# Performance work log

Measured on AMD Instinct MI355X. Metric: run time of the kernel, lower is better.

The kernel has to match this reference:

```python
import jax, jax.numpy as jnp
import numpy as np

B, NQ, K = 256, 16, 200           # batch, num_neg+1, num_keys
KEY_SIZE, QUERY_SIZE, HIDDEN = 64, 64, 128
NEG_INF_SCALE = -1000000000.0


def setup_inputs() -> dict:
    key = jax.random.key(0)
    ks = jax.random.split(key, 9)
    queries = jax.random.normal(ks[0], (B, NQ, QUERY_SIZE), dtype=jnp.float32)
    keys = jax.random.normal(ks[1], (B, K, KEY_SIZE), dtype=jnp.float32)
    cum_subs_masks = (jax.random.uniform(ks[2], (B, NQ, K, 1)) < 0.3).astype(jnp.float32)
    s = 1.0 / np.sqrt(HIDDEN)
    Wq = jax.random.normal(ks[3], (QUERY_SIZE, HIDDEN), dtype=jnp.float32) * s
    bq = jnp.zeros((HIDDEN,), dtype=jnp.float32)
    Wk = jax.random.normal(ks[4], (KEY_SIZE, HIDDEN), dtype=jnp.float32) * s
    bk = jnp.zeros((HIDDEN,), dtype=jnp.float32)
    Wv = jax.random.normal(ks[5], (HIDDEN, 1), dtype=jnp.float32) * s
    bv = jnp.zeros((1,), dtype=jnp.float32)
    return {"queries": queries, "keys": keys, "cum_subs_masks": cum_subs_masks,
            "num_neg": NQ - 1, "Wq": Wq, "bq": bq, "Wk": Wk, "bk": bk,
            "Wv": Wv, "bv": bv}


def reference(queries, keys, cum_subs_masks, num_neg, Wq, bq, Wk, bk, Wv, bv):
    # project once, broadcast instead of expanding keys per query (same math)
    qh = queries @ Wq + bq                 # (B, NQ, H)
    kh = keys @ Wk + bk                    # (B, K, H)
    h = jnp.tanh(qh[:, :, None, :] + kh[:, None, :, :])   # (B, NQ, K, H)
    scores = h @ Wv + bv                   # (B, NQ, K, 1)
    if cum_subs_masks is not None:
        scores = scores + cum_subs_masks * NEG_INF_SCALE
    attn_weight = jax.nn.softmax(scores, axis=-2)          # softmax over keys
    attn_out = jnp.sum(attn_weight * keys[:, None, :, :], axis=-2)  # (B, NQ, key_size)
    return (attn_out, attn_weight)
```

## Files before the change

### kernel.cpp

```cpp
#include <hip/hip_runtime.h>
#include <hip/hip_bf16.h>

namespace {

typedef __attribute__((ext_vector_type(8))) short short8;
typedef __attribute__((ext_vector_type(4))) float f32x4;

constexpr int kNB = 256;
constexpr int kNQ = 16;
constexpr int kNK = 200;
constexpr int kDK = 64;
constexpr int kNH = 128;
constexpr int kThreads = 1024;
constexpr int kS = 132;
constexpr float kNeg = -1000000000.0f;
constexpr float kC2 = 2.8853900817779268f;

constexpr int kKhFloats = kNK * kS;
constexpr int kScFloats = kNQ * kNK;
constexpr int kQhFloats = kNQ * kNH;
constexpr size_t kSmemBytes =
    (size_t)(kKhFloats + kScFloats + kQhFloats) * sizeof(float);

__device__ __forceinline__ float exp2_hw(float x) {
#if defined(__has_builtin)
# if __has_builtin(__builtin_amdgcn_exp2f)
  return __builtin_amdgcn_exp2f(x);
# else
  return __expf(x * 0.69314718055994531f);
# endif
#else
  return __expf(x * 0.69314718055994531f);
#endif
}

template <int CTRL>
__device__ __forceinline__ float dpp_add(float v) {
  int sw = __builtin_amdgcn_update_dpp(0, __float_as_int(v), CTRL, 0xF, 0xF, true);
  return v + __int_as_float(sw);
}

__device__ __forceinline__ void split8(float4 a, float4 b, short8& hi, short8& lo) {
  float v[8] = {a.x, a.y, a.z, a.w, b.x, b.y, b.z, b.w};
#pragma unroll
  for (int j = 0; j < 8; ++j) {
    const __hip_bfloat16 h = __float2bfloat16(v[j]);
    hi[j] = (short)__bfloat16_as_ushort(h);
    const __hip_bfloat16 l = __float2bfloat16(v[j] - __bfloat162float(h));
    lo[j] = (short)__bfloat16_as_ushort(l);
  }
}

__launch_bounds__(kThreads)
__attribute__((amdgpu_waves_per_eu(4, 4)))
__global__ void bahdanau_fused(const float* __restrict__ queries,
                               const float* __restrict__ keys,
                               const float* __restrict__ masks,
                               const float* __restrict__ Wq,
                               const float* __restrict__ bq,
                               const float* __restrict__ Wk,
                               const float* __restrict__ bk,
                               const float* __restrict__ Wv,
                               float* __restrict__ out_attn,
                               float* __restrict__ out_w) {
  extern __shared__ __align__(16) float smem[];
  float* skh = smem;
  float* ssc = smem + kKhFloats;
  float* sqh = smem + kKhFloats + kScFloats;

  const int tid  = threadIdx.x;
  const int b    = blockIdx.x;
  const int lane = tid & 63;
  const int wave = __builtin_amdgcn_readfirstlane(tid >> 6);
  const int l15  = lane & 15;
  const int q16  = lane >> 4;
  const int hbase = 8 * l15;

  const float* kb = keys + (size_t)b * kNK * kDK;
  const float* qb = queries + (size_t)b * kNQ * kDK;

  {
    const int tc  = wave >> 1;
    const int odd = wave & 1;
    const int col = tc * 16 + l15;
    const int kj0 = q16 * 8;

    short8 bh[2], bl[2];
#pragma unroll
    for (int p = 0; p < 2; ++p) {
      float4 v0, v1;
      v0.x = Wk[(p * 32 + kj0 + 0) * kNH + col];
      v0.y = Wk[(p * 32 + kj0 + 1) * kNH + col];
      v0.z = Wk[(p * 32 + kj0 + 2) * kNH + col];
      v0.w = Wk[(p * 32 + kj0 + 3) * kNH + col];
      v1.x = Wk[(p * 32 + kj0 + 4) * kNH + col];
      v1.y = Wk[(p * 32 + kj0 + 5) * kNH + col];
      v1.z = Wk[(p * 32 + kj0 + 6) * kNH + col];
      v1.w = Wk[(p * 32 + kj0 + 7) * kNH + col];
      split8(v0, v1, bh[p], bl[p]);
    }
    const float bkc = bk[col];

    const int trB = odd ? 7 : 0;
    const int trE = odd ? 13 : 7;
    for (int tr = trB; tr < trE; ++tr) {
      f32x4 acc = {0.f, 0.f, 0.f, 0.f};
      const int row = tr * 16 + l15;
      const bool ok = row < kNK;
#pragma unroll
      for (int p = 0; p < 2; ++p) {
        float4 a0 = {0.f, 0.f, 0.f, 0.f}, a1 = {0.f, 0.f, 0.f, 0.f};
        if (ok) {
          const float* ap = kb + (size_t)row * kDK + p * 32 + kj0;
          a0 = *reinterpret_cast<const float4*>(ap);
          a1 = *reinterpret_cast<const float4*>(ap + 4);
        }
        short8 ah, al;
        split8(a0, a1, ah, al);
        acc = __builtin_amdgcn_mfma_f32_16x16x32_bf16(al, bh[p], acc, 0, 0, 0);
        acc = __builtin_amdgcn_mfma_f32_16x16x32_bf16(ah, bl[p], acc, 0, 0, 0);
        acc = __builtin_amdgcn_mfma_f32_16x16x32_bf16(ah, bh[p], acc, 0, 0, 0);
      }
#pragma unroll
      for (int r = 0; r < 4; ++r) {
        const int rr = tr * 16 + q16 * 4 + r;
        if (rr < kNK) skh[(size_t)rr * kS + col] = exp2_hw(kC2 * (acc[r] + bkc));
      }
    }

    if (odd) {
      short8 qbh[2], qbl[2];
#pragma unroll
      for (int p = 0; p < 2; ++p) {
        float4 v0, v1;
        v0.x = Wq[(p * 32 + kj0 + 0) * kNH + col];
        v0.y = Wq[(p * 32 + kj0 + 1) * kNH + col];
        v0.z = Wq[(p * 32 + kj0 + 2) * kNH + col];
        v0.w = Wq[(p * 32 + kj0 + 3) * kNH + col];
        v1.x = Wq[(p * 32 + kj0 + 4) * kNH + col];
        v1.y = Wq[(p * 32 + kj0 + 5) * kNH + col];
        v1.z = Wq[(p * 32 + kj0 + 6) * kNH + col];
        v1.w = Wq[(p * 32 + kj0 + 7) * kNH + col];
        split8(v0, v1, qbh[p], qbl[p]);
      }
      const float bqc = bq[col];
      f32x4 acc = {0.f, 0.f, 0.f, 0.f};
#pragma unroll
      for (int p = 0; p < 2; ++p) {
        const float* ap = qb + (size_t)l15 * kDK + p * 32 + kj0;
        const float4 a0 = *reinterpret_cast<const float4*>(ap);
        const float4 a1 = *reinterpret_cast<const float4*>(ap + 4);
        short8 ah, al;
        split8(a0, a1, ah, al);
        acc = __builtin_amdgcn_mfma_f32_16x16x32_bf16(al, qbh[p], acc, 0, 0, 0);
        acc = __builtin_amdgcn_mfma_f32_16x16x32_bf16(ah, qbl[p], acc, 0, 0, 0);
        acc = __builtin_amdgcn_mfma_f32_16x16x32_bf16(ah, qbh[p], acc, 0, 0, 0);
      }
#pragma unroll
      for (int r = 0; r < 4; ++r)
        sqh[(size_t)(q16 * 4 + r) * kNH + col] = exp2_hw(kC2 * (acc[r] + bqc));
    }
  }

  float wv2[8];
  {
    const float4 wva = *reinterpret_cast<const float4*>(&Wv[hbase]);
    const float4 wvb = *reinterpret_cast<const float4*>(&Wv[hbase + 4]);
    wv2[0] = -2.0f * wva.x; wv2[1] = -2.0f * wva.y;
    wv2[2] = -2.0f * wva.z; wv2[3] = -2.0f * wva.w;
    wv2[4] = -2.0f * wvb.x; wv2[5] = -2.0f * wvb.y;
    wv2[6] = -2.0f * wvb.z; wv2[7] = -2.0f * wvb.w;
  }

  const float* mrow = masks + ((size_t)b * kNQ + wave) * kNK;
  const bool tail = lane < (kNK - 192);
  const float mm0 = mrow[lane];
  const float mm1 = mrow[lane + 64];
  const float mm2 = mrow[lane + 128];
  const float mm3 = tail ? mrow[lane + 192] : 0.0f;

  __syncthreads();

  const int qg = wave >> 2;
  const int kg = wave & 3;
  float qreg[4][8];
#pragma unroll
  for (int qi = 0; qi < 4; ++qi) {
    const float4 qa  = *reinterpret_cast<const float4*>(&sqh[(4 * qg + qi) * kNH + hbase]);
    const float4 qb4 = *reinterpret_cast<const float4*>(&sqh[(4 * qg + qi) * kNH + hbase + 4]);
    qreg[qi][0] = qa.x;  qreg[qi][1] = qa.y;  qreg[qi][2] = qa.z;  qreg[qi][3] = qa.w;
    qreg[qi][4] = qb4.x; qreg[qi][5] = qb4.y; qreg[qi][6] = qb4.z; qreg[qi][7] = qb4.w;
  }
#pragma unroll
  for (int qi = 0; qi < 4; ++qi)
#pragma unroll
    for (int m = 0; m < 8; ++m) asm volatile("" : "+v"(qreg[qi][m]));

  {
    auto score_k = [&](int k) {
      const float* krow = &skh[(size_t)k * kS + hbase];
      const float4 ka  = *reinterpret_cast<const float4*>(krow);
      const float4 kb4 = *reinterpret_cast<const float4*>(krow + 4);
#pragma unroll
      for (int qi = 0; qi < 4; ++qi) {
        const float uA = fmaf(qreg[qi][0], ka.x, 1.0f);
        const float vA = fmaf(qreg[qi][1], ka.y, 1.0f);
        const float wA = fmaf(qreg[qi][2], ka.z, 1.0f);
        const float xA = fmaf(qreg[qi][3], ka.w, 1.0f);
        const float p1A = uA * vA;
        const float p2A = wA * xA;
        const float n1A = fmaf(wv2[0], vA, wv2[1] * uA);
        const float n2A = fmaf(wv2[2], xA, wv2[3] * wA);
        const float denA = p1A * p2A;
        const float numA = fmaf(n1A, p2A, n2A * p1A);
        const float uB = fmaf(qreg[qi][4], kb4.x, 1.0f);
        const float vB = fmaf(qreg[qi][5], kb4.y, 1.0f);
        const float wB = fmaf(qreg[qi][6], kb4.z, 1.0f);
        const float xB = fmaf(qreg[qi][7], kb4.w, 1.0f);
        const float p1B = uB * vB;
        const float p2B = wB * xB;
        const float n1B = fmaf(wv2[4], vB, wv2[5] * uB);
        const float n2B = fmaf(wv2[6], xB, wv2[7] * wB);
        const float denB = p1B * p2B;
        const float numB = fmaf(n1B, p2B, n2B * p1B);
        const float rA = __builtin_amdgcn_rcpf(denA);
        const float rB = __builtin_amdgcn_rcpf(denB);
        float acc = fmaf(numB, rB, numA * rA);
        acc = dpp_add<0xB1>(acc);
        acc = dpp_add<0x4E>(acc);
        acc = dpp_add<0x141>(acc);
        acc = dpp_add<0x140>(acc);
        if (l15 == 0) ssc[(4 * qg + qi) * kNK + k] = acc;
      }
    };
    for (int i = 0; i < 12; ++i) score_k(16 * i + 4 * kg + q16);
    if (kg < 2) score_k(192 + 4 * kg + q16);
  }

  __syncthreads();

  {
    const float* sr = &ssc[wave * kNK];
    const float e0 = __expf(fmaf(mm0, kNeg, sr[lane]));
    const float e1 = __expf(fmaf(mm1, kNeg, sr[lane + 64]));
    const float e2 = __expf(fmaf(mm2, kNeg, sr[lane + 128]));
    const float e3 = tail ? __expf(fmaf(mm3, kNeg, sr[lane + 192])) : 0.f;
    float sum = (e0 + e1) + (e2 + e3);
#pragma unroll
    for (int off = 32; off > 0; off >>= 1) sum += __shfl_xor(sum, off, 64);
    const float rs = __builtin_amdgcn_rcpf(sum);
    float* og = out_w + ((size_t)b * kNQ + wave) * kNK;
    float* swr = &ssc[wave * kNK];
    const float w0 = e0 * rs, w1 = e1 * rs, w2 = e2 * rs, w3 = e3 * rs;
    swr[lane]       = w0;  og[lane]       = w0;
    swr[lane + 64]  = w1;  og[lane + 64]  = w1;
    swr[lane + 128] = w2;  og[lane + 128] = w2;
    if (tail) { swr[lane + 192] = w3; og[lane + 192] = w3; }
  }
  __syncthreads();

  {
    float* pk = skh;
    const int kstart = 52 * kg;
    const int kend = (kg == 3) ? kNK : (kstart + 52);
    const float* kb2 = kb + lane;
    float acc[4] = {0.f, 0.f, 0.f, 0.f};
    for (int k0 = kstart; k0 < kend; k0 += 4) {
      const float kv0 = kb2[(size_t)(k0 + 0) * kDK];
      const float kv1 = kb2[(size_t)(k0 + 1) * kDK];
      const float kv2 = kb2[(size_t)(k0 + 2) * kDK];
      const float kv3 = kb2[(size_t)(k0 + 3) * kDK];
#pragma unroll
      for (int qi = 0; qi < 4; ++qi) {
        const float4 wq = *reinterpret_cast<const float4*>(&ssc[(4 * qg + qi) * kNK + k0]);
        acc[qi] = fmaf(wq.x, kv0, acc[qi]);
        acc[qi] = fmaf(wq.y, kv1, acc[qi]);
        acc[qi] = fmaf(wq.z, kv2, acc[qi]);
        acc[qi] = fmaf(wq.w, kv3, acc[qi]);
      }
    }
#pragma unroll
    for (int qi = 0; qi < 4; ++qi)
      pk[((4 * qg + qi) * 4 + kg) * kDK + lane] = acc[qi];
  }
  __syncthreads();

  {
    const float* pk = skh;
    const float r = pk[(wave * 4 + 0) * kDK + lane] + pk[(wave * 4 + 1) * kDK + lane] +
                    pk[(wave * 4 + 2) * kDK + lane] + pk[(wave * 4 + 3) * kDK + lane];
    out_attn[((size_t)b * kNQ + wave) * kDK + lane] = r;
  }
}

}

extern "C" void kernel_launch(void* const* d_in, const int* in_sizes, int n_in,
                              void* d_out, int out_size, void* d_ws, size_t ws_size,
                              hipStream_t stream) {
  const float* queries = (const float*)d_in[0];
  const float* keys    = (const float*)d_in[1];
  const float* masks   = (const float*)d_in[2];
  const float* Wq = (const float*)d_in[4];
  const float* bq = (const float*)d_in[5];
  const float* Wk = (const float*)d_in[6];
  const float* bk = (const float*)d_in[7];
  const float* Wv = (const float*)d_in[8];

  float* out_attn = (float*)d_out;
  float* out_w    = out_attn + (size_t)kNB * kNQ * kDK;

  hipFuncSetAttribute((const void*)bahdanau_fused,
                      hipFuncAttributeMaxDynamicSharedMemorySize, (int)kSmemBytes);
  bahdanau_fused<<<kNB, kThreads, kSmemBytes, stream>>>(queries, keys, masks, Wq, bq,
                                                        Wk, bk, Wv, out_attn, out_w);
}
```

Baseline: 35.98 us.

## Split key projection into halves and overlap second half with scoring

Key projection is split into two halves of 100 rows. The first half is projected before the barrier, and the second half's MFMA projection runs while waves compute scores for the first half. This hides part of the projection latency behind the VALU-heavy scoring phase, at the cost of an extra block-wide barrier and some changes to load balancing.

```diff
diff --git a/kernel.cpp b/kernel.cpp
--- a/kernel.cpp
+++ b/kernel.cpp
@@ -9,14 +9,16 @@
 constexpr int kNB = 256;
 constexpr int kNQ = 16;
 constexpr int kNK = 200;
+constexpr int kHK = 100;
 constexpr int kDK = 64;
 constexpr int kNH = 128;
 constexpr int kThreads = 1024;
 constexpr int kS = 132;
+constexpr int kHalfFloats = kHK * kS;
 constexpr float kNeg = -1000000000.0f;
 constexpr float kC2 = 2.8853900817779268f;
 
-constexpr int kKhFloats = kNK * kS;
+constexpr int kKhFloats = 2 * kHalfFloats;
 constexpr int kScFloats = kNQ * kNK;
 constexpr int kQhFloats = kNQ * kNH;
 constexpr size_t kSmemBytes =
@@ -79,87 +81,88 @@
   const float* kb = keys + (size_t)b * kNK * kDK;
   const float* qb = queries + (size_t)b * kNQ * kDK;
 
-  {
-    const int tc  = wave >> 1;
-    const int odd = wave & 1;
-    const int col = tc * 16 + l15;
-    const int kj0 = q16 * 8;
-
-    short8 bh[2], bl[2];
+  const int tc  = wave >> 1;
+  const int odd = wave & 1;
+  const int col = tc * 16 + l15;
+  const int kj0 = q16 * 8;
+
+  short8 bh[2], bl[2];
+#pragma unroll
+  for (int p = 0; p < 2; ++p) {
+    float4 v0, v1;
+    v0.x = Wk[(p * 32 + kj0 + 0) * kNH + col];
+    v0.y = Wk[(p * 32 + kj0 + 1) * kNH + col];
+    v0.z = Wk[(p * 32 + kj0 + 2) * kNH + col];
+    v0.w = Wk[(p * 32 + kj0 + 3) * kNH + col];
+    v1.x = Wk[(p * 32 + kj0 + 4) * kNH + col];
+    v1.y = Wk[(p * 32 + kj0 + 5) * kNH + col];
+    v1.z = Wk[(p * 32 + kj0 + 6) * kNH + col];
+    v1.w = Wk[(p * 32 + kj0 + 7) * kNH + col];
+    split8(v0, v1, bh[p], bl[p]);
+  }
+  const float bkc = bk[col];
+
+  auto proj_tile = [&](int half, int t) {
+    f32x4 acc = {0.f, 0.f, 0.f, 0.f};
+    const int rl = t * 16 + l15;
+    const bool ok = rl < kHK;
+    const float* kbh = kb + (size_t)half * kHK * kDK;
+#pragma unroll
+    for (int p = 0; p < 2; ++p) {
+      float4 a0 = {0.f, 0.f, 0.f, 0.f}, a1 = {0.f, 0.f, 0.f, 0.f};
+      if (ok) {
+        const float* ap = kbh + (size_t)rl * kDK + p * 32 + kj0;
+        a0 = *reinterpret_cast<const float4*>(ap);
+        a1 = *reinterpret_cast<const float4*>(ap + 4);
+      }
+      short8 ah, al;
+      split8(a0, a1, ah, al);
+      acc = __builtin_amdgcn_mfma_f32_16x16x32_bf16(al, bh[p], acc, 0, 0, 0);
+      acc = __builtin_amdgcn_mfma_f32_16x16x32_bf16(ah, bl[p], acc, 0, 0, 0);
+      acc = __builtin_amdgcn_mfma_f32_16x16x32_bf16(ah, bh[p], acc, 0, 0, 0);
+    }
+#pragma unroll
+    for (int r = 0; r < 4; ++r) {
+      const int rr = t * 16 + q16 * 4 + r;
+      if (rr < kHK) skh[half * kHalfFloats + rr * kS + col] =
+          exp2_hw(kC2 * (acc[r] + bkc));
+    }
+  };
+
+  if (!odd) {
+    proj_tile(0, 0); proj_tile(0, 1); proj_tile(0, 2); proj_tile(0, 3);
+  } else {
+    proj_tile(0, 4); proj_tile(0, 5); proj_tile(0, 6);
+    short8 qbh[2], qbl[2];
 #pragma unroll
     for (int p = 0; p < 2; ++p) {
       float4 v0, v1;
-      v0.x = Wk[(p * 32 + kj0 + 0) * kNH + col];
-      v0.y = Wk[(p * 32 + kj0 + 1) * kNH + col];
-      v0.z = Wk[(p * 32 + kj0 + 2) * kNH + col];
-      v0.w = Wk[(p * 32 + kj0 + 3) * kNH + col];
-      v1.x = Wk[(p * 32 + kj0 + 4) * kNH + col];
-      v1.y = Wk[(p * 32 + kj0 + 5) * kNH + col];
-      v1.z = Wk[(p * 32 + kj0 + 6) * kNH + col];
-      v1.w = Wk[(p * 32 + kj0 + 7) * kNH + col];
-      split8(v0, v1, bh[p], bl[p]);
-    }
-    const float bkc = bk[col];
-
-    const int trB = odd ? 7 : 0;
-    const int trE = odd ? 13 : 7;
-    for (int tr = trB; tr < trE; ++tr) {
-      f32x4 acc = {0.f, 0.f, 0.f, 0.f};
-      const int row = tr * 16 + l15;
-      const bool ok = row < kNK;
-#pragma unroll
-      for (int p = 0; p < 2; ++p) {
-        float4 a0 = {0.f, 0.f, 0.f, 0.f}, a1 = {0.f, 0.f, 0.f, 0.f};
-        if (ok) {
-          const float* ap = kb + (size_t)row * kDK + p * 32 + kj0;
-          a0 = *reinterpret_cast<const float4*>(ap);
-          a1 = *reinterpret_cast<const float4*>(ap + 4);
-        }
-        short8 ah, al;
-        split8(a0, a1, ah, al);
-        acc = __builtin_amdgcn_mfma_f32_16x16x32_bf16(al, bh[p], acc, 0, 0, 0);
-        acc = __builtin_amdgcn_mfma_f32_16x16x32_bf16(ah, bl[p], acc, 0, 0, 0);
-        acc = __builtin_amdgcn_mfma_f32_16x16x32_bf16(ah, bh[p], acc, 0, 0, 0);
-      }
-#pragma unroll
-      for (int r = 0; r < 4; ++r) {
-        const int rr = tr * 16 + q16 * 4 + r;
-        if (rr < kNK) skh[(size_t)rr * kS + col] = exp2_hw(kC2 * (acc[r] + bkc));
-      }
-    }
-
-    if (odd) {
-      short8 qbh[2], qbl[2];
-#pragma unroll
-      for (int p = 0; p < 2; ++p) {
-        float4 v0, v1;
-        v0.x = Wq[(p * 32 + kj0 + 0) * kNH + col];
-        v0.y = Wq[(p * 32 + kj0 + 1) * kNH + col];
-        v0.z = Wq[(p * 32 + kj0 + 2) * kNH + col];
-        v0.w = Wq[(p * 32 + kj0 + 3) * kNH + col];
-        v1.x = Wq[(p * 32 + kj0 + 4) * kNH + col];
-        v1.y = Wq[(p * 32 + kj0 + 5) * kNH + col];
-        v1.z = Wq[(p * 32 + kj0 + 6) * kNH + col];
-        v1.w = Wq[(p * 32 + kj0 + 7) * kNH + col];
-        split8(v0, v1, qbh[p], qbl[p]);
-      }
-      const float bqc = bq[col];
-      f32x4 acc = {0.f, 0.f, 0.f, 0.f};
-#pragma unroll
-      for (int p = 0; p < 2; ++p) {
-        const float* ap = qb + (size_t)l15 * kDK + p * 32 + kj0;
-        const float4 a0 = *reinterpret_cast<const float4*>(ap);
-        const float4 a1 = *reinterpret_cast<const float4*>(ap + 4);
-        short8 ah, al;
-        split8(a0, a1, ah, al);
-        acc = __builtin_amdgcn_mfma_f32_16x16x32_bf16(al, qbh[p], acc, 0, 0, 0);
-        acc = __builtin_amdgcn_mfma_f32_16x16x32_bf16(ah, qbl[p], acc, 0, 0, 0);
-        acc = __builtin_amdgcn_mfma_f32_16x16x32_bf16(ah, qbh[p], acc, 0, 0, 0);
-      }
-#pragma unroll
-      for (int r = 0; r < 4; ++r)
-        sqh[(size_t)(q16 * 4 + r) * kNH + col] = exp2_hw(kC2 * (acc[r] + bqc));
-    }
+      v0.x = Wq[(p * 32 + kj0 + 0) * kNH + col];
+      v0.y = Wq[(p * 32 + kj0 + 1) * kNH + col];
+      v0.z = Wq[(p * 32 + kj0 + 2) * kNH + col];
+      v0.w = Wq[(p * 32 + kj0 + 3) * kNH + col];
+      v1.x = Wq[(p * 32 + kj0 + 4) * kNH + col];
+      v1.y = Wq[(p * 32 + kj0 + 5) * kNH + col];
+      v1.z = Wq[(p * 32 + kj0 + 6) * kNH + col];
+      v1.w = Wq[(p * 32 + kj0 + 7) * kNH + col];
+      split8(v0, v1, qbh[p], qbl[p]);
+    }
+    const float bqc = bq[col];
+    f32x4 acc = {0.f, 0.f, 0.f, 0.f};
+#pragma unroll
+    for (int p = 0; p < 2; ++p) {
+      const float* ap = qb + (size_t)l15 * kDK + p * 32 + kj0;
+      const float4 a0 = *reinterpret_cast<const float4*>(ap);
+      const float4 a1 = *reinterpret_cast<const float4*>(ap + 4);
+      short8 ah, al;
+      split8(a0, a1, ah, al);
+      acc = __builtin_amdgcn_mfma_f32_16x16x32_bf16(al, qbh[p], acc, 0, 0, 0);
+      acc = __builtin_amdgcn_mfma_f32_16x16x32_bf16(ah, qbl[p], acc, 0, 0, 0);
+      acc = __builtin_amdgcn_mfma_f32_16x16x32_bf16(ah, qbh[p], acc, 0, 0, 0);
+    }
+#pragma unroll
+    for (int r = 0; r < 4; ++r)
+      sqh[(size_t)(q16 * 4 + r) * kNH + col] = exp2_hw(kC2 * (acc[r] + bqc));
   }
 
   float wv2[8];
@@ -196,46 +199,56 @@
 #pragma unroll
     for (int m = 0; m < 8; ++m) asm volatile("" : "+v"(qreg[qi][m]));
 
-  {
-    auto score_k = [&](int k) {
-      const float* krow = &skh[(size_t)k * kS + hbase];
-      const float4 ka  = *reinterpret_cast<const float4*>(krow);
-      const float4 kb4 = *reinterpret_cast<const float4*>(krow + 4);
-#pragma unroll
-      for (int qi = 0; qi < 4; ++qi) {
-        const float uA = fmaf(qreg[qi][0], ka.x, 1.0f);
-        const float vA = fmaf(qreg[qi][1], ka.y, 1.0f);
-        const float wA = fmaf(qreg[qi][2], ka.z, 1.0f);
-        const float xA = fmaf(qreg[qi][3], ka.w, 1.0f);
-        const float p1A = uA * vA;
-        const float p2A = wA * xA;
-        const float n1A = fmaf(wv2[0], vA, wv2[1] * uA);
-        const float n2A = fmaf(wv2[2], xA, wv2[3] * wA);
-        const float denA = p1A * p2A;
-        const float numA = fmaf(n1A, p2A, n2A * p1A);
-        const float uB = fmaf(qreg[qi][4], kb4.x, 1.0f);
-        const float vB = fmaf(qreg[qi][5], kb4.y, 1.0f);
-        const float wB = fmaf(qreg[qi][6], kb4.z, 1.0f);
-        const float xB = fmaf(qreg[qi][7], kb4.w, 1.0f);
-        const float p1B = uB * vB;
-        const float p2B = wB * xB;
-        const float n1B = fmaf(wv2[4], vB, wv2[5] * uB);
-        const float n2B = fmaf(wv2[6], xB, wv2[7] * wB);
-        const float denB = p1B * p2B;
-        const float numB = fmaf(n1B, p2B, n2B * p1B);
-        const float rA = __builtin_amdgcn_rcpf(denA);
-        const float rB = __builtin_amdgcn_rcpf(denB);
-        float acc = fmaf(numB, rB, numA * rA);
-        acc = dpp_add<0xB1>(acc);
-        acc = dpp_add<0x4E>(acc);
-        acc = dpp_add<0x141>(acc);
-        acc = dpp_add<0x140>(acc);
-        if (l15 == 0) ssc[(4 * qg + qi) * kNK + k] = acc;
-      }
-    };
-    for (int i = 0; i < 12; ++i) score_k(16 * i + 4 * kg + q16);
-    if (kg < 2) score_k(192 + 4 * kg + q16);
-  }
+  auto score_k = [&](int half, int klocal) {
+    const float* krow = &skh[half * kHalfFloats + klocal * kS + hbase];
+    const float4 ka  = *reinterpret_cast<const float4*>(krow);
+    const float4 kb4 = *reinterpret_cast<const float4*>(krow + 4);
+    const int k = half * kHK + klocal;
+#pragma unroll
+    for (int qi = 0; qi < 4; ++qi) {
+      const float uA = fmaf(qreg[qi][0], ka.x, 1.0f);
+      const float vA = fmaf(qreg[qi][1], ka.y, 1.0f);
+      const float wA = fmaf(qreg[qi][2], ka.z, 1.0f);
+      const float xA = fmaf(qreg[qi][3], ka.w, 1.0f);
+      const float p1A = uA * vA;
+      const float p2A = wA * xA;
+      const float n1A = fmaf(wv2[0], vA, wv2[1] * uA);
+      const float n2A = fmaf(wv2[2], xA, wv2[3] * wA);
+      const float denA = p1A * p2A;
+      const float numA = fmaf(n1A, p2A, n2A * p1A);
+      const float uB = fmaf(qreg[qi][4], kb4.x, 1.0f);
+      const float vB = fmaf(qreg[qi][5], kb4.y, 1.0f);
+      const float wB = fmaf(qreg[qi][6], kb4.z, 1.0f);
+      const float xB = fmaf(qreg[qi][7], kb4.w, 1.0f);
+      const float p1B = uB * vB;
+      const float p2B = wB * xB;
+      const float n1B = fmaf(wv2[4], vB, wv2[5] * uB);
+      const float n2B = fmaf(wv2[6], xB, wv2[7] * wB);
+      const float denB = p1B * p2B;
+      const float numB = fmaf(n1B, p2B, n2B * p1B);
+      const float rA = __builtin_amdgcn_rcpf(denA);
+      const float rB = __builtin_amdgcn_rcpf(denB);
+      float acc = fmaf(numB, rB, numA * rA);
+      acc = dpp_add<0xB1>(acc);
+      acc = dpp_add<0x4E>(acc);
+      acc = dpp_add<0x141>(acc);
+      acc = dpp_add<0x140>(acc);
+      if (l15 == 0) ssc[(4 * qg + qi) * kNK + k] = acc;
+    }
+  };
+
+  if (!odd) {
+    proj_tile(1, 0); proj_tile(1, 1); proj_tile(1, 2); proj_tile(1, 3);
+  } else {
+    proj_tile(1, 4); proj_tile(1, 5); proj_tile(1, 6);
+  }
+  for (int i = 0; i < 6; ++i) score_k(0, 16 * i + 4 * kg + q16);
+  if (kg == 0) score_k(0, 96 + q16);
+
+  __syncthreads();
+
+  for (int i = 0; i < 6; ++i) score_k(1, 16 * i + 4 * kg + q16);
+  if (kg == 0) score_k(1, 96 + q16);
 
   __syncthreads();
 
```

New measurement: 37.36 us. +3.8%, slower.
